# Kernel optimization log

Hardware: AMD Instinct MI355X
Metric: run time of the kernel (lower is better)

The kernel has to match this reference:

```python
import jax, jax.numpy as jnp
import numpy as np

B, LQ, LK = 4, 2048, 2048
DQ, DC = 1024, 1024
H, DH = 16, 64
INNER = H * DH
LN_EPS = 1e-5
TAU_INIT = DH ** -0.5


def layernorm(x, w, b):
    mu = jnp.mean(x, axis=-1, keepdims=True)
    var = jnp.var(x, axis=-1, keepdims=True)
    return (x - mu) * jax.lax.rsqrt(var + LN_EPS) * w + b


def l2norm(x, eps=1e-12):
    # matches F.normalize(dim=-1): x / max(||x||, eps)
    n = jnp.sqrt(jnp.sum(x * x, axis=-1, keepdims=True))
    return x / jnp.maximum(n, eps)


def setup_inputs() -> dict:
    key = jax.random.key(0)
    ks = jax.random.split(key, 8)
    s = lambda d: (1.0 / np.sqrt(d)).astype(np.float32) if isinstance(d, np.ndarray) else np.float32(1.0 / np.sqrt(d))
    return {
        "x": jax.random.normal(ks[0], (B, LQ, DQ), jnp.float32),
        "context": jax.random.normal(ks[1], (B, LK, DC), jnp.float32),
        "key_padding_mask": jax.random.bernoulli(ks[2], 0.1, (B, LK)),
        "ln_q_w": jnp.ones((DQ,), jnp.float32),
        "ln_q_b": jnp.zeros((DQ,), jnp.float32),
        "ln_ctx_w": jnp.ones((DC,), jnp.float32),
        "ln_ctx_b": jnp.zeros((DC,), jnp.float32),
        "Wq": jax.random.normal(ks[3], (DQ, INNER), jnp.float32) * s(DQ),
        "Wk": jax.random.normal(ks[4], (DC, INNER), jnp.float32) * s(DC),
        "Wv": jax.random.normal(ks[5], (DC, INNER), jnp.float32) * s(DC),
        "Wo": jax.random.normal(ks[6], (INNER, DQ), jnp.float32) * s(INNER),
        "tau": jnp.float32(TAU_INIT),
    }


def reference(x, context, key_padding_mask, ln_q_w, ln_q_b, ln_ctx_w, ln_ctx_b, Wq, Wk, Wv, Wo, tau):
    q_in = layernorm(x, ln_q_w, ln_q_b)
    kv_in = layernorm(context, ln_ctx_w, ln_ctx_b)
    q = (q_in @ Wq).reshape(B, LQ, H, DH)   # [B,Lq,H,Dh]
    k = (kv_in @ Wk).reshape(B, LK, H, DH)
    v = (kv_in @ Wv).reshape(B, LK, H, DH)
    q = l2norm(q)
    k = l2norm(k)
    scores = jnp.einsum('bqhd,bkhd->bhqk', q, k) / (tau + 1e-6)
    scores = jnp.where(key_padding_mask[:, None, None, :], -jnp.inf, scores)
    attn = jax.nn.softmax(scores, axis=-1)
    out = jnp.einsum('bhqk,bkhd->bqhd', attn, v).reshape(B, LQ, INNER)
    return out @ Wo
```

## Files before the change

### kernel.cpp

```cpp
#include <hip/hip_runtime.h>

typedef unsigned short u16;
typedef __bf16 bf16x8 __attribute__((ext_vector_type(8)));
typedef short s16x4 __attribute__((ext_vector_type(4)));
typedef float f32x4 __attribute__((ext_vector_type(4)));

__device__ __forceinline__ u16 f2bf(float f) {
  unsigned u = __float_as_uint(f);
  unsigned r = u + 0x7fffu + ((u >> 16) & 1u);
  return (u16)(r >> 16);
}

__device__ __forceinline__ unsigned cvt_pk(float a, float b) {
  unsigned r;
  asm("v_cvt_pk_bf16_f32 %0, %1, %2" : "=v"(r) : "v"(a), "v"(b));
  return r;
}

__device__ __forceinline__ void async_cp16(const void* g, void* l) {
  __builtin_amdgcn_global_load_lds((__attribute__((address_space(1))) void*)g,
                                   (__attribute__((address_space(3))) void*)l,
                                   16, 0, 0);
}

#define MFMA32(a, b, c) __builtin_amdgcn_mfma_f32_16x16x32_bf16(a, b, c, 0, 0, 0)

#if __has_builtin(__builtin_amdgcn_mfma_f32_16x16x16bf16_1k)
#define MFMA16(a, b, c) __builtin_amdgcn_mfma_f32_16x16x16bf16_1k(a, b, c, 0, 0, 0)
#else
__device__ __forceinline__ f32x4 mfma16_fb(s16x4 a, s16x4 b, f32x4 c) {
  asm("v_mfma_f32_16x16x16_bf16 %0, %1, %2, %0" : "+v"(c) : "v"(a), "v"(b));
  return c;
}
#define MFMA16(a, b, c) mfma16_fb(a, b, c)
#endif

__global__ __launch_bounds__(256)
void ln_cast(const float* __restrict__ X, const float* __restrict__ W,
             const float* __restrict__ Bv, u16* __restrict__ Y) {
  __shared__ float red[8];
  const int row = blockIdx.x, t = threadIdx.x;
  const int wave = t >> 6, lane = t & 63;
  const float4 v = ((const float4*)(X + (size_t)row * 1024))[t];
  float s  = v.x + v.y + v.z + v.w;
  float ss = v.x*v.x + v.y*v.y + v.z*v.z + v.w*v.w;
#pragma unroll
  for (int m = 32; m; m >>= 1) { s += __shfl_xor(s, m, 64); ss += __shfl_xor(ss, m, 64); }
  if (lane == 0) { red[wave] = s; red[4 + wave] = ss; }
  __syncthreads();
  float S  = red[0] + red[1] + red[2] + red[3];
  float SS = red[4] + red[5] + red[6] + red[7];
  float mu  = S * (1.0f / 1024.0f);
  float var = SS * (1.0f / 1024.0f) - mu * mu;
  float rstd = rsqrtf(var + 1e-5f);
  const float4 wv = ((const float4*)W)[t];
  const float4 bv = ((const float4*)Bv)[t];
  ushort4 o;
  o.x = f2bf((v.x - mu) * rstd * wv.x + bv.x);
  o.y = f2bf((v.y - mu) * rstd * wv.y + bv.y);
  o.z = f2bf((v.z - mu) * rstd * wv.z + bv.z);
  o.w = f2bf((v.w - mu) * rstd * wv.w + bv.w);
  ((ushort4*)(Y + (size_t)row * 1024))[t] = o;
}

__global__ __launch_bounds__(256)
void wtrans(const float* __restrict__ W, u16* __restrict__ WT) {
  __shared__ float t[64][65];
  const int k0 = blockIdx.y * 64, n0 = blockIdx.x * 64;
  const int lr = threadIdx.x >> 4, lc = threadIdx.x & 15;
#pragma unroll
  for (int r = 0; r < 4; ++r) {
    int row = r * 16 + lr;
    float4 v = *(const float4*)(W + (size_t)(k0 + row) * 1024 + n0 + lc * 4);
    t[row][lc*4+0] = v.x; t[row][lc*4+1] = v.y; t[row][lc*4+2] = v.z; t[row][lc*4+3] = v.w;
  }
  __syncthreads();
#pragma unroll
  for (int r = 0; r < 4; ++r) {
    int n = r * 16 + lr;
    ushort4 o;
    o.x = f2bf(t[lc*4+0][n]); o.y = f2bf(t[lc*4+1][n]);
    o.z = f2bf(t[lc*4+2][n]); o.w = f2bf(t[lc*4+3][n]);
    *(ushort4*)(WT + (size_t)(n0 + n) * 1024 + k0 + lc * 4) = o;
  }
}

__global__ __launch_bounds__(256)
void vtrans(const float* __restrict__ V, u16* __restrict__ VT) {
  __shared__ float t[64][65];
  const int b = blockIdx.z, h = blockIdx.y, kk0 = blockIdx.x * 64;
  const int lr = threadIdx.x >> 4, lc = threadIdx.x & 15;
#pragma unroll
  for (int r = 0; r < 4; ++r) {
    int row = r * 16 + lr;
    float4 v = *(const float4*)(V + (size_t)(b * 2048 + kk0 + row) * 1024 + h * 64 + lc * 4);
    t[row][lc*4+0] = v.x; t[row][lc*4+1] = v.y; t[row][lc*4+2] = v.z; t[row][lc*4+3] = v.w;
  }
  __syncthreads();
#pragma unroll
  for (int r = 0; r < 4; ++r) {
    int d = r * 16 + lr;
    ushort4 o;
    o.x = f2bf(t[lc*4+0][d]); o.y = f2bf(t[lc*4+1][d]);
    o.z = f2bf(t[lc*4+2][d]); o.w = f2bf(t[lc*4+3][d]);
    *(ushort4*)(VT + ((size_t)(b * 16 + h) * 64 + d) * 2048 + kk0 + lc * 4) = o;
  }
}

__global__ __launch_bounds__(256, 2)
void gemm_bt(const u16* __restrict__ A, const u16* __restrict__ Bt,
             float* __restrict__ C, int M, int N, int K) {
  __shared__ __align__(16) u16 As[128 * 64];
  __shared__ __align__(16) u16 Bs[128 * 64];
  const int tid = threadIdx.x;
  const int wave = tid >> 6, lane = tid & 63;
  const int quad = lane >> 4, l15 = lane & 15;
  const int m0 = blockIdx.y * 128, n0 = blockIdx.x * 128;
  const int wm = (wave >> 1) * 64, wn = (wave & 1) * 64;
  const int srow = lane >> 3, scol = (lane & 7) * 8;

  const f32x4 fz = {0.f, 0.f, 0.f, 0.f};
  f32x4 acc[4][4];
#pragma unroll
  for (int i = 0; i < 4; ++i)
#pragma unroll
    for (int j = 0; j < 4; ++j) acc[i][j] = fz;

  for (int kt = 0; kt < K; kt += 64) {
    __syncthreads();
#pragma unroll
    for (int r = 0; r < 4; ++r) {
      const int c = r * 4 + wave;
      const int row = c * 8 + srow;
      async_cp16(A  + (size_t)(m0 + row) * K + kt + scol, (char*)As + c * 1024);
      async_cp16(Bt + (size_t)(n0 + row) * K + kt + scol, (char*)Bs + c * 1024);
    }
    __syncthreads();
#pragma unroll
    for (int ks = 0; ks < 2; ++ks) {
      bf16x8 af[4], bfr[4];
#pragma unroll
      for (int i = 0; i < 4; ++i)
        af[i] = *(const bf16x8*)(const void*)(As + (wm + i * 16 + l15) * 64 + ks * 32 + quad * 8);
#pragma unroll
      for (int j = 0; j < 4; ++j)
        bfr[j] = *(const bf16x8*)(const void*)(Bs + (wn + j * 16 + l15) * 64 + ks * 32 + quad * 8);
#pragma unroll
      for (int i = 0; i < 4; ++i)
#pragma unroll
        for (int j = 0; j < 4; ++j)
          acc[i][j] = MFMA32(af[i], bfr[j], acc[i][j]);
    }
  }
#pragma unroll
  for (int i = 0; i < 4; ++i)
#pragma unroll
    for (int j = 0; j < 4; ++j)
#pragma unroll
      for (int e = 0; e < 4; ++e) {
        int row = m0 + wm + i * 16 + quad * 4 + e;
        int col = n0 + wn + j * 16 + l15;
        C[(size_t)row * N + col] = acc[i][j][e];
      }
}

__global__ __launch_bounds__(256, 2)
void gemm_l2n(const u16* __restrict__ A, const u16* __restrict__ Bt,
              u16* __restrict__ Y, const float* __restrict__ taup, int scaled) {
  __shared__ __align__(16) u16 As[128 * 64];
  __shared__ __align__(16) u16 Bs[128 * 64];
  const int tid = threadIdx.x;
  const int wave = tid >> 6, lane = tid & 63;
  const int quad = lane >> 4, l15 = lane & 15;
  const int m0 = blockIdx.y * 128, n0 = blockIdx.x * 128;
  const int wm = (wave >> 1) * 64, wn = (wave & 1) * 64;
  const int srow = lane >> 3, scol = (lane & 7) * 8;
  const int K = 1024, N = 1024;

  const f32x4 fz = {0.f, 0.f, 0.f, 0.f};
  f32x4 acc[4][4];
#pragma unroll
  for (int i = 0; i < 4; ++i)
#pragma unroll
    for (int j = 0; j < 4; ++j) acc[i][j] = fz;

  for (int kt = 0; kt < K; kt += 64) {
    __syncthreads();
#pragma unroll
    for (int r = 0; r < 4; ++r) {
      const int c = r * 4 + wave;
      const int row = c * 8 + srow;
      async_cp16(A  + (size_t)(m0 + row) * K + kt + scol, (char*)As + c * 1024);
      async_cp16(Bt + (size_t)(n0 + row) * K + kt + scol, (char*)Bs + c * 1024);
    }
    __syncthreads();
#pragma unroll
    for (int ks = 0; ks < 2; ++ks) {
      bf16x8 af[4], bfr[4];
#pragma unroll
      for (int i = 0; i < 4; ++i)
        af[i] = *(const bf16x8*)(const void*)(As + (wm + i * 16 + l15) * 64 + ks * 32 + quad * 8);
#pragma unroll
      for (int j = 0; j < 4; ++j)
        bfr[j] = *(const bf16x8*)(const void*)(Bs + (wn + j * 16 + l15) * 64 + ks * 32 + quad * 8);
#pragma unroll
      for (int i = 0; i < 4; ++i)
#pragma unroll
        for (int j = 0; j < 4; ++j)
          acc[i][j] = MFMA32(af[i], bfr[j], acc[i][j]);
    }
  }
  const float tsc = scaled ? 1.44269504f / (taup[0] + 1e-6f) : 1.0f;
#pragma unroll
  for (int i = 0; i < 4; ++i)
#pragma unroll
    for (int e = 0; e < 4; ++e) {
      float ss = 0.f;
#pragma unroll
      for (int j = 0; j < 4; ++j) ss = fmaf(acc[i][j][e], acc[i][j][e], ss);
      ss += __shfl_xor(ss, 1, 64); ss += __shfl_xor(ss, 2, 64);
      ss += __shfl_xor(ss, 4, 64); ss += __shfl_xor(ss, 8, 64);
      float sc = tsc / fmaxf(sqrtf(ss), 1e-12f);
      int row = m0 + wm + i * 16 + quad * 4 + e;
#pragma unroll
      for (int j = 0; j < 4; ++j)
        Y[(size_t)row * N + n0 + wn + j * 16 + l15] = f2bf(acc[i][j][e] * sc);
    }
}

__global__ __launch_bounds__(256, 2)
void flash_attn6(const u16* __restrict__ Qb, const u16* __restrict__ Kb,
                 const u16* __restrict__ Vt, const int* __restrict__ mask,
                 u16* __restrict__ Ob) {
  __shared__ __align__(16) u16 QPs[256 * 64];
  __shared__ __align__(16) u16 Ks[64 * 64];
  __shared__ __align__(16) u16 Vs[64 * 64];
  __shared__ __align__(16) u16 Msb[2048];
  const int tid = threadIdx.x, w = tid >> 6, lane = tid & 63;
  const int quad = lane >> 4, l15 = lane & 15;
  const int b = blockIdx.z, h = blockIdx.y, q0 = blockIdx.x * 256;
  const int srow = lane >> 3;
  const int scolX = ((lane & 7) ^ srow) * 8;
  const int fsw = ((l15 & 7) << 4);

#pragma unroll
  for (int r = 0; r < 8; ++r) {
    int c = w * 8 + r;
    async_cp16(Qb + (size_t)(b * 2048 + q0 + c * 8 + srow) * 1024 + h * 64 + scolX,
               (char*)QPs + c * 1024);
  }
  {
    const int* mp = mask + b * 2048 + tid * 8;
    int4 ma = *(const int4*)mp;
    int4 mb = *(const int4*)(mp + 4);
    ushort4 o0, o1;
    o0.x = ma.x ? 0xFF7Fu : 0u; o0.y = ma.y ? 0xFF7Fu : 0u;
    o0.z = ma.z ? 0xFF7Fu : 0u; o0.w = ma.w ? 0xFF7Fu : 0u;
    o1.x = mb.x ? 0xFF7Fu : 0u; o1.y = mb.y ? 0xFF7Fu : 0u;
    o1.z = mb.z ? 0xFF7Fu : 0u; o1.w = mb.w ? 0xFF7Fu : 0u;
    *(ushort4*)(Msb + tid * 8)     = o0;
    *(ushort4*)(Msb + tid * 8 + 4) = o1;
  }
  __syncthreads();

  bf16x8 aq[4][2];
#pragma unroll
  for (int i = 0; i < 4; ++i)
#pragma unroll
    for (int ks = 0; ks < 2; ++ks)
      aq[i][ks] = *(const bf16x8*)(const void*)(
          (const char*)QPs + (w * 64 + i * 16 + l15) * 128 + (((ks * 4 + quad) << 4) ^ fsw));

  const f32x4 fz = {0.f, 0.f, 0.f, 0.f};
  f32x4 o[4][4];
  float rs[4] = {0.f, 0.f, 0.f, 0.f};
#pragma unroll
  for (int dt = 0; dt < 4; ++dt)
#pragma unroll
    for (int i = 0; i < 4; ++i) o[dt][i] = fz;

  for (int kt = 0; kt < 2048; kt += 64) {
    __syncthreads();
#pragma unroll
    for (int r = 0; r < 2; ++r) {
      int c = w * 2 + r;
      async_cp16(Kb + (size_t)(b * 2048 + kt + c * 8 + srow) * 1024 + h * 64 + scolX,
                 (char*)Ks + c * 1024);
      async_cp16(Vt + ((size_t)(b * 16 + h) * 64 + c * 8 + srow) * 2048 + kt + scolX,
                 (char*)Vs + c * 1024);
    }
    __syncthreads();

    bf16x8 kb[4][2];
#pragma unroll
    for (int kkt = 0; kkt < 4; ++kkt)
#pragma unroll
      for (int ks = 0; ks < 2; ++ks)
        kb[kkt][ks] = *(const bf16x8*)(const void*)(
            (const char*)Ks + (kkt * 16 + l15) * 128 + (((ks * 4 + quad) << 4) ^ fsw));

#pragma unroll
    for (int kkt = 0; kkt < 4; ++kkt) {
      s16x4 mbv = *(const s16x4*)(Msb + kt + kkt * 16 + quad * 4);
      f32x4 bias;
#pragma unroll
      for (int e = 0; e < 4; ++e)
        bias[e] = __uint_as_float(((unsigned)(u16)mbv[e]) << 16);

      s16x4 pf[4];
#pragma unroll
      for (int i = 0; i < 4; ++i) {
        f32x4 st = MFMA32(kb[kkt][0], aq[i][0], bias);
        st = MFMA32(kb[kkt][1], aq[i][1], st);
        float p0 = exp2f(st[0]), p1 = exp2f(st[1]);
        float p2 = exp2f(st[2]), p3 = exp2f(st[3]);
        rs[i] += (p0 + p1) + (p2 + p3);
        union { unsigned u[2]; s16x4 s; } pk;
        pk.u[0] = cvt_pk(p0, p1);
        pk.u[1] = cvt_pk(p2, p3);
        pf[i] = pk.s;
      }
      __builtin_amdgcn_s_setprio(1);
#pragma unroll
      for (int dt = 0; dt < 4; ++dt) {
        s16x4 va = *(const s16x4*)(const void*)(
            (const char*)Vs + (dt * 16 + l15) * 128 + ((kkt * 32 + quad * 8) ^ fsw));
#pragma unroll
        for (int i = 0; i < 4; ++i)
          o[dt][i] = MFMA16(va, pf[i], o[dt][i]);
      }
      __builtin_amdgcn_s_setprio(0);
    }
  }

  float inv[4];
#pragma unroll
  for (int i = 0; i < 4; ++i) {
    float v = rs[i];
    v += __shfl_xor(v, 16, 64);
    v += __shfl_xor(v, 32, 64);
    inv[i] = 1.0f / v;
  }

  u16* strip = QPs + w * 64 * 64;
#pragma unroll
  for (int dt = 0; dt < 4; ++dt)
#pragma unroll
    for (int i = 0; i < 4; ++i) {
      union { unsigned u[2]; s16x4 s; } pk;
      pk.u[0] = cvt_pk(o[dt][i][0] * inv[i], o[dt][i][1] * inv[i]);
      pk.u[1] = cvt_pk(o[dt][i][2] * inv[i], o[dt][i][3] * inv[i]);
      *(s16x4*)(void*)((char*)strip + (i * 16 + l15) * 128 + ((dt * 32 + quad * 8) ^ fsw)) = pk.s;
    }
#pragma unroll
  for (int pass = 0; pass < 8; ++pass) {
    int row = pass * 8 + (lane >> 3), oct = lane & 7;
    int4 v = *(const int4*)(const void*)((const char*)strip + row * 128 + ((oct ^ (row & 7)) << 4));
    *(int4*)(Ob + (size_t)(b * 2048 + q0 + w * 64 + row) * 1024 + h * 64 + oct * 8) = v;
  }
}

extern "C" void kernel_launch(void* const* d_in, const int* in_sizes, int n_in,
                              void* d_out, int out_size, void* d_ws, size_t ws_size,
                              hipStream_t stream) {
  const float* x    = (const float*)d_in[0];
  const float* ctx  = (const float*)d_in[1];
  const int*   mask = (const int*)d_in[2];
  const float* lnqw = (const float*)d_in[3];
  const float* lnqb = (const float*)d_in[4];
  const float* lncw = (const float*)d_in[5];
  const float* lncb = (const float*)d_in[6];
  const float* Wq   = (const float*)d_in[7];
  const float* Wk   = (const float*)d_in[8];
  const float* Wv   = (const float*)d_in[9];
  const float* Wo   = (const float*)d_in[10];
  const float* tau  = (const float*)d_in[11];
  float* out = (float*)d_out;
  char* ws = (char*)d_ws;
  const size_t MB = 1024 * 1024;

  u16* qin  = (u16*)(ws + 0 * MB);
  u16* kvin = (u16*)(ws + 16 * MB);
  u16* WqT  = (u16*)(ws + 32 * MB);
  u16* WkT  = (u16*)(ws + 34 * MB);
  u16* WvT  = (u16*)(ws + 36 * MB);
  u16* WoT  = (u16*)(ws + 38 * MB);
  u16* qbf  = (u16*)(ws + 40 * MB);
  u16* kbf  = (u16*)(ws + 56 * MB);
  u16* vT   = (u16*)(ws + 72 * MB);
  float* scr = out;
  u16* attn = qin;

  ln_cast<<<8192, 256, 0, stream>>>(x,   lnqw, lnqb, qin);
  ln_cast<<<8192, 256, 0, stream>>>(ctx, lncw, lncb, kvin);
  wtrans<<<dim3(16, 16), 256, 0, stream>>>(Wq, WqT);
  wtrans<<<dim3(16, 16), 256, 0, stream>>>(Wk, WkT);
  wtrans<<<dim3(16, 16), 256, 0, stream>>>(Wv, WvT);
  wtrans<<<dim3(16, 16), 256, 0, stream>>>(Wo, WoT);

  gemm_l2n<<<dim3(8, 64), 256, 0, stream>>>(qin,  WqT, qbf, tau, 1);
  gemm_l2n<<<dim3(8, 64), 256, 0, stream>>>(kvin, WkT, kbf, tau, 0);

  gemm_bt<<<dim3(8, 64), 256, 0, stream>>>(kvin, WvT, scr, 8192, 1024, 1024);
  vtrans<<<dim3(32, 16, 4), 256, 0, stream>>>(scr, vT);

  flash_attn6<<<dim3(8, 16, 4), 256, 0, stream>>>(qbf, kbf, vT, mask, attn);

  gemm_bt<<<dim3(8, 64), 256, 0, stream>>>(attn, WoT, out, 8192, 1024, 1024);
}
```

Measured before the change: 394.5 us.

## Double-buffer LDS tiles in GEMM and flash-attention kernels to overlap loads

The projection GEMMs and the attention kernel now keep two LDS buffers per operand. Each loop iteration issues the async global-to-LDS copy for the next tile before computing on the current one. This leaves a single barrier per iteration instead of two, so global load latency can hide behind MFMA work. In exchange, LDS use per block doubles for the operand tiles, which could limit occupancy. Correctness also depends on the barrier waiting for the async LDS copies to complete.

After: 404.2 us. +2.5%, slower.

```diff
diff --git a/kernel.cpp b/kernel.cpp
--- a/kernel.cpp
+++ b/kernel.cpp
@@ -110,8 +110,8 @@
 __global__ __launch_bounds__(256, 2)
 void gemm_bt(const u16* __restrict__ A, const u16* __restrict__ Bt,
              float* __restrict__ C, int M, int N, int K) {
-  __shared__ __align__(16) u16 As[128 * 64];
-  __shared__ __align__(16) u16 Bs[128 * 64];
+  __shared__ __align__(16) u16 As[2][128 * 64];
+  __shared__ __align__(16) u16 Bs[2][128 * 64];
   const int tid = threadIdx.x;
   const int wave = tid >> 6, lane = tid & 63;
   const int quad = lane >> 4, l15 = lane & 15;
@@ -126,31 +126,43 @@
 #pragma unroll
     for (int j = 0; j < 4; ++j) acc[i][j] = fz;
 
+#pragma unroll
+  for (int r = 0; r < 4; ++r) {
+    const int c = r * 4 + wave;
+    const int row = c * 8 + srow;
+    async_cp16(A  + (size_t)(m0 + row) * K + scol, (char*)As[0] + c * 1024);
+    async_cp16(Bt + (size_t)(n0 + row) * K + scol, (char*)Bs[0] + c * 1024);
+  }
+  __syncthreads();
+
+  int cur = 0;
   for (int kt = 0; kt < K; kt += 64) {
-    __syncthreads();
-#pragma unroll
-    for (int r = 0; r < 4; ++r) {
-      const int c = r * 4 + wave;
-      const int row = c * 8 + srow;
-      async_cp16(A  + (size_t)(m0 + row) * K + kt + scol, (char*)As + c * 1024);
-      async_cp16(Bt + (size_t)(n0 + row) * K + kt + scol, (char*)Bs + c * 1024);
-    }
-    __syncthreads();
+    if (kt + 64 < K) {
+#pragma unroll
+      for (int r = 0; r < 4; ++r) {
+        const int c = r * 4 + wave;
+        const int row = c * 8 + srow;
+        async_cp16(A  + (size_t)(m0 + row) * K + kt + 64 + scol, (char*)As[cur ^ 1] + c * 1024);
+        async_cp16(Bt + (size_t)(n0 + row) * K + kt + 64 + scol, (char*)Bs[cur ^ 1] + c * 1024);
+      }
+    }
 #pragma unroll
     for (int ks = 0; ks < 2; ++ks) {
       bf16x8 af[4], bfr[4];
 #pragma unroll
       for (int i = 0; i < 4; ++i)
-        af[i] = *(const bf16x8*)(const void*)(As + (wm + i * 16 + l15) * 64 + ks * 32 + quad * 8);
+        af[i] = *(const bf16x8*)(const void*)(As[cur] + (wm + i * 16 + l15) * 64 + ks * 32 + quad * 8);
 #pragma unroll
       for (int j = 0; j < 4; ++j)
-        bfr[j] = *(const bf16x8*)(const void*)(Bs + (wn + j * 16 + l15) * 64 + ks * 32 + quad * 8);
+        bfr[j] = *(const bf16x8*)(const void*)(Bs[cur] + (wn + j * 16 + l15) * 64 + ks * 32 + quad * 8);
 #pragma unroll
       for (int i = 0; i < 4; ++i)
 #pragma unroll
         for (int j = 0; j < 4; ++j)
           acc[i][j] = MFMA32(af[i], bfr[j], acc[i][j]);
     }
+    __syncthreads();
+    cur ^= 1;
   }
 #pragma unroll
   for (int i = 0; i < 4; ++i)
@@ -167,8 +179,8 @@
 __global__ __launch_bounds__(256, 2)
 void gemm_l2n(const u16* __restrict__ A, const u16* __restrict__ Bt,
               u16* __restrict__ Y, const float* __restrict__ taup, int scaled) {
-  __shared__ __align__(16) u16 As[128 * 64];
-  __shared__ __align__(16) u16 Bs[128 * 64];
+  __shared__ __align__(16) u16 As[2][128 * 64];
+  __shared__ __align__(16) u16 Bs[2][128 * 64];
   const int tid = threadIdx.x;
   const int wave = tid >> 6, lane = tid & 63;
   const int quad = lane >> 4, l15 = lane & 15;
@@ -184,31 +196,43 @@
 #pragma unroll
     for (int j = 0; j < 4; ++j) acc[i][j] = fz;
 
+#pragma unroll
+  for (int r = 0; r < 4; ++r) {
+    const int c = r * 4 + wave;
+    const int row = c * 8 + srow;
+    async_cp16(A  + (size_t)(m0 + row) * K + scol, (char*)As[0] + c * 1024);
+    async_cp16(Bt + (size_t)(n0 + row) * K + scol, (char*)Bs[0] + c * 1024);
+  }
+  __syncthreads();
+
+  int cur = 0;
   for (int kt = 0; kt < K; kt += 64) {
-    __syncthreads();
-#pragma unroll
-    for (int r = 0; r < 4; ++r) {
-      const int c = r * 4 + wave;
-      const int row = c * 8 + srow;
-      async_cp16(A  + (size_t)(m0 + row) * K + kt + scol, (char*)As + c * 1024);
-      async_cp16(Bt + (size_t)(n0 + row) * K + kt + scol, (char*)Bs + c * 1024);
-    }
-    __syncthreads();
+    if (kt + 64 < K) {
+#pragma unroll
+      for (int r = 0; r < 4; ++r) {
+        const int c = r * 4 + wave;
+        const int row = c * 8 + srow;
+        async_cp16(A  + (size_t)(m0 + row) * K + kt + 64 + scol, (char*)As[cur ^ 1] + c * 1024);
+        async_cp16(Bt + (size_t)(n0 + row) * K + kt + 64 + scol, (char*)Bs[cur ^ 1] + c * 1024);
+      }
+    }
 #pragma unroll
     for (int ks = 0; ks < 2; ++ks) {
       bf16x8 af[4], bfr[4];
 #pragma unroll
       for (int i = 0; i < 4; ++i)
-        af[i] = *(const bf16x8*)(const void*)(As + (wm + i * 16 + l15) * 64 + ks * 32 + quad * 8);
+        af[i] = *(const bf16x8*)(const void*)(As[cur] + (wm + i * 16 + l15) * 64 + ks * 32 + quad * 8);
 #pragma unroll
       for (int j = 0; j < 4; ++j)
-        bfr[j] = *(const bf16x8*)(const void*)(Bs + (wn + j * 16 + l15) * 64 + ks * 32 + quad * 8);
+        bfr[j] = *(const bf16x8*)(const void*)(Bs[cur] + (wn + j * 16 + l15) * 64 + ks * 32 + quad * 8);
 #pragma unroll
       for (int i = 0; i < 4; ++i)
 #pragma unroll
         for (int j = 0; j < 4; ++j)
           acc[i][j] = MFMA32(af[i], bfr[j], acc[i][j]);
     }
+    __syncthreads();
+    cur ^= 1;
   }
   const float tsc = scaled ? 1.44269504f / (taup[0] + 1e-6f) : 1.0f;
 #pragma unroll
@@ -229,12 +253,12 @@
 }
 
 __global__ __launch_bounds__(256, 2)
-void flash_attn6(const u16* __restrict__ Qb, const u16* __restrict__ Kb,
+void flash_attn7(const u16* __restrict__ Qb, const u16* __restrict__ Kb,
                  const u16* __restrict__ Vt, const int* __restrict__ mask,
                  u16* __restrict__ Ob) {
   __shared__ __align__(16) u16 QPs[256 * 64];
-  __shared__ __align__(16) u16 Ks[64 * 64];
-  __shared__ __align__(16) u16 Vs[64 * 64];
+  __shared__ __align__(16) u16 Ks[2][64 * 64];
+  __shared__ __align__(16) u16 Vs[2][64 * 64];
   __shared__ __align__(16) u16 Msb[2048];
   const int tid = threadIdx.x, w = tid >> 6, lane = tid & 63;
   const int quad = lane >> 4, l15 = lane & 15;
@@ -248,6 +272,14 @@
     int c = w * 8 + r;
     async_cp16(Qb + (size_t)(b * 2048 + q0 + c * 8 + srow) * 1024 + h * 64 + scolX,
                (char*)QPs + c * 1024);
+  }
+#pragma unroll
+  for (int r = 0; r < 2; ++r) {
+    int c = w * 2 + r;
+    async_cp16(Kb + (size_t)(b * 2048 + c * 8 + srow) * 1024 + h * 64 + scolX,
+               (char*)Ks[0] + c * 1024);
+    async_cp16(Vt + ((size_t)(b * 16 + h) * 64 + c * 8 + srow) * 2048 + scolX,
+               (char*)Vs[0] + c * 1024);
   }
   {
     const int* mp = mask + b * 2048 + tid * 8;
@@ -279,17 +311,18 @@
 #pragma unroll
     for (int i = 0; i < 4; ++i) o[dt][i] = fz;
 
+  int cur = 0;
   for (int kt = 0; kt < 2048; kt += 64) {
-    __syncthreads();
-#pragma unroll
-    for (int r = 0; r < 2; ++r) {
-      int c = w * 2 + r;
-      async_cp16(Kb + (size_t)(b * 2048 + kt + c * 8 + srow) * 1024 + h * 64 + scolX,
-                 (char*)Ks + c * 1024);
-      async_cp16(Vt + ((size_t)(b * 16 + h) * 64 + c * 8 + srow) * 2048 + kt + scolX,
-                 (char*)Vs + c * 1024);
-    }
-    __syncthreads();
+    if (kt + 64 < 2048) {
+#pragma unroll
+      for (int r = 0; r < 2; ++r) {
+        int c = w * 2 + r;
+        async_cp16(Kb + (size_t)(b * 2048 + kt + 64 + c * 8 + srow) * 1024 + h * 64 + scolX,
+                   (char*)Ks[cur ^ 1] + c * 1024);
+        async_cp16(Vt + ((size_t)(b * 16 + h) * 64 + c * 8 + srow) * 2048 + kt + 64 + scolX,
+                   (char*)Vs[cur ^ 1] + c * 1024);
+      }
+    }
 
     bf16x8 kb[4][2];
 #pragma unroll
@@ -297,7 +330,7 @@
 #pragma unroll
       for (int ks = 0; ks < 2; ++ks)
         kb[kkt][ks] = *(const bf16x8*)(const void*)(
-            (const char*)Ks + (kkt * 16 + l15) * 128 + (((ks * 4 + quad) << 4) ^ fsw));
+            (const char*)Ks[cur] + (kkt * 16 + l15) * 128 + (((ks * 4 + quad) << 4) ^ fsw));
 
 #pragma unroll
     for (int kkt = 0; kkt < 4; ++kkt) {
@@ -324,13 +357,15 @@
 #pragma unroll
       for (int dt = 0; dt < 4; ++dt) {
         s16x4 va = *(const s16x4*)(const void*)(
-            (const char*)Vs + (dt * 16 + l15) * 128 + ((kkt * 32 + quad * 8) ^ fsw));
+            (const char*)Vs[cur] + (dt * 16 + l15) * 128 + ((kkt * 32 + quad * 8) ^ fsw));
 #pragma unroll
         for (int i = 0; i < 4; ++i)
           o[dt][i] = MFMA16(va, pf[i], o[dt][i]);
       }
       __builtin_amdgcn_s_setprio(0);
     }
+    __syncthreads();
+    cur ^= 1;
   }
 
   float inv[4];
@@ -404,7 +439,7 @@
   gemm_bt<<<dim3(8, 64), 256, 0, stream>>>(kvin, WvT, scr, 8192, 1024, 1024);
   vtrans<<<dim3(32, 16, 4), 256, 0, stream>>>(scr, vT);
 
-  flash_attn6<<<dim3(8, 16, 4), 256, 0, stream>>>(qbf, kbf, vT, mask, attn);
+  flash_attn7<<<dim3(8, 16, 4), 256, 0, stream>>>(qbf, kbf, vT, mask, attn);
 
   gemm_bt<<<dim3(8, 64), 256, 0, stream>>>(attn, WoT, out, 8192, 1024, 1024);
 }
```

## Double-buffer K/V tiles in attention, use fp32 mask bias and fast exp2

Applied to the files above, without the earlier changes.

The attention kernel now prefetches the next K/V tile into a second LDS buffer while the current tile is being computed, replacing the two barriers per iteration with one. The mask bias is stored as fp32 in LDS, so it is read directly and no longer unpacked from bf16. exp2f is swapped for the hardware exp2 builtin. The added LDS for the double buffers and the mask may reduce occupancy, and there is a possible race because there is no wait on the async loads before the tile is read.

Measured after the change: 366.6 us. -7.1%, faster.

```diff
diff --git a/kernel.cpp b/kernel.cpp
--- a/kernel.cpp
+++ b/kernel.cpp
@@ -16,6 +16,12 @@
   asm("v_cvt_pk_bf16_f32 %0, %1, %2" : "=v"(r) : "v"(a), "v"(b));
   return r;
 }
+
+#if __has_builtin(__builtin_amdgcn_exp2f)
+#define EXP2(x) __builtin_amdgcn_exp2f(x)
+#else
+#define EXP2(x) exp2f(x)
+#endif
 
 __device__ __forceinline__ void async_cp16(const void* g, void* l) {
   __builtin_amdgcn_global_load_lds((__attribute__((address_space(1))) void*)g,
@@ -229,13 +235,13 @@
 }
 
 __global__ __launch_bounds__(256, 2)
-void flash_attn6(const u16* __restrict__ Qb, const u16* __restrict__ Kb,
+void flash_attn9(const u16* __restrict__ Qb, const u16* __restrict__ Kb,
                  const u16* __restrict__ Vt, const int* __restrict__ mask,
                  u16* __restrict__ Ob) {
   __shared__ __align__(16) u16 QPs[256 * 64];
-  __shared__ __align__(16) u16 Ks[64 * 64];
-  __shared__ __align__(16) u16 Vs[64 * 64];
-  __shared__ __align__(16) u16 Msb[2048];
+  __shared__ __align__(16) u16 Ks[2][64 * 64];
+  __shared__ __align__(16) u16 Vs[2][64 * 64];
+  __shared__ __align__(16) float Msf[2048];
   const int tid = threadIdx.x, w = tid >> 6, lane = tid & 63;
   const int quad = lane >> 4, l15 = lane & 15;
   const int b = blockIdx.z, h = blockIdx.y, q0 = blockIdx.x * 256;
@@ -249,17 +255,25 @@
     async_cp16(Qb + (size_t)(b * 2048 + q0 + c * 8 + srow) * 1024 + h * 64 + scolX,
                (char*)QPs + c * 1024);
   }
+#pragma unroll
+  for (int r = 0; r < 2; ++r) {
+    int c = w * 2 + r;
+    async_cp16(Kb + (size_t)(b * 2048 + c * 8 + srow) * 1024 + h * 64 + scolX,
+               (char*)Ks[0] + c * 1024);
+    async_cp16(Vt + ((size_t)(b * 16 + h) * 64 + c * 8 + srow) * 2048 + scolX,
+               (char*)Vs[0] + c * 1024);
+  }
   {
     const int* mp = mask + b * 2048 + tid * 8;
     int4 ma = *(const int4*)mp;
     int4 mb = *(const int4*)(mp + 4);
-    ushort4 o0, o1;
-    o0.x = ma.x ? 0xFF7Fu : 0u; o0.y = ma.y ? 0xFF7Fu : 0u;
-    o0.z = ma.z ? 0xFF7Fu : 0u; o0.w = ma.w ? 0xFF7Fu : 0u;
-    o1.x = mb.x ? 0xFF7Fu : 0u; o1.y = mb.y ? 0xFF7Fu : 0u;
-    o1.z = mb.z ? 0xFF7Fu : 0u; o1.w = mb.w ? 0xFF7Fu : 0u;
-    *(ushort4*)(Msb + tid * 8)     = o0;
-    *(ushort4*)(Msb + tid * 8 + 4) = o1;
+    float4 o0, o1;
+    o0.x = ma.x ? -3.0e38f : 0.f; o0.y = ma.y ? -3.0e38f : 0.f;
+    o0.z = ma.z ? -3.0e38f : 0.f; o0.w = ma.w ? -3.0e38f : 0.f;
+    o1.x = mb.x ? -3.0e38f : 0.f; o1.y = mb.y ? -3.0e38f : 0.f;
+    o1.z = mb.z ? -3.0e38f : 0.f; o1.w = mb.w ? -3.0e38f : 0.f;
+    *(float4*)(Msf + tid * 8)     = o0;
+    *(float4*)(Msf + tid * 8 + 4) = o1;
   }
   __syncthreads();
 
@@ -279,17 +293,18 @@
 #pragma unroll
     for (int i = 0; i < 4; ++i) o[dt][i] = fz;
 
+  int cur = 0;
   for (int kt = 0; kt < 2048; kt += 64) {
-    __syncthreads();
-#pragma unroll
-    for (int r = 0; r < 2; ++r) {
-      int c = w * 2 + r;
-      async_cp16(Kb + (size_t)(b * 2048 + kt + c * 8 + srow) * 1024 + h * 64 + scolX,
-                 (char*)Ks + c * 1024);
-      async_cp16(Vt + ((size_t)(b * 16 + h) * 64 + c * 8 + srow) * 2048 + kt + scolX,
-                 (char*)Vs + c * 1024);
-    }
-    __syncthreads();
+    if (kt + 64 < 2048) {
+#pragma unroll
+      for (int r = 0; r < 2; ++r) {
+        int c = w * 2 + r;
+        async_cp16(Kb + (size_t)(b * 2048 + kt + 64 + c * 8 + srow) * 1024 + h * 64 + scolX,
+                   (char*)Ks[cur ^ 1] + c * 1024);
+        async_cp16(Vt + ((size_t)(b * 16 + h) * 64 + c * 8 + srow) * 2048 + kt + 64 + scolX,
+                   (char*)Vs[cur ^ 1] + c * 1024);
+      }
+    }
 
     bf16x8 kb[4][2];
 #pragma unroll
@@ -297,23 +312,19 @@
 #pragma unroll
       for (int ks = 0; ks < 2; ++ks)
         kb[kkt][ks] = *(const bf16x8*)(const void*)(
-            (const char*)Ks + (kkt * 16 + l15) * 128 + (((ks * 4 + quad) << 4) ^ fsw));
+            (const char*)Ks[cur] + (kkt * 16 + l15) * 128 + (((ks * 4 + quad) << 4) ^ fsw));
 
 #pragma unroll
     for (int kkt = 0; kkt < 4; ++kkt) {
-      s16x4 mbv = *(const s16x4*)(Msb + kt + kkt * 16 + quad * 4);
-      f32x4 bias;
-#pragma unroll
-      for (int e = 0; e < 4; ++e)
-        bias[e] = __uint_as_float(((unsigned)(u16)mbv[e]) << 16);
+      f32x4 bias = *(const f32x4*)(Msf + kt + kkt * 16 + quad * 4);
 
       s16x4 pf[4];
 #pragma unroll
       for (int i = 0; i < 4; ++i) {
         f32x4 st = MFMA32(kb[kkt][0], aq[i][0], bias);
         st = MFMA32(kb[kkt][1], aq[i][1], st);
-        float p0 = exp2f(st[0]), p1 = exp2f(st[1]);
-        float p2 = exp2f(st[2]), p3 = exp2f(st[3]);
+        float p0 = EXP2(st[0]), p1 = EXP2(st[1]);
+        float p2 = EXP2(st[2]), p3 = EXP2(st[3]);
         rs[i] += (p0 + p1) + (p2 + p3);
         union { unsigned u[2]; s16x4 s; } pk;
         pk.u[0] = cvt_pk(p0, p1);
@@ -324,13 +335,15 @@
 #pragma unroll
       for (int dt = 0; dt < 4; ++dt) {
         s16x4 va = *(const s16x4*)(const void*)(
-            (const char*)Vs + (dt * 16 + l15) * 128 + ((kkt * 32 + quad * 8) ^ fsw));
+            (const char*)Vs[cur] + (dt * 16 + l15) * 128 + ((kkt * 32 + quad * 8) ^ fsw));
 #pragma unroll
         for (int i = 0; i < 4; ++i)
           o[dt][i] = MFMA16(va, pf[i], o[dt][i]);
       }
       __builtin_amdgcn_s_setprio(0);
     }
+    __syncthreads();
+    cur ^= 1;
   }
 
   float inv[4];
@@ -404,7 +417,7 @@
   gemm_bt<<<dim3(8, 64), 256, 0, stream>>>(kvin, WvT, scr, 8192, 1024, 1024);
   vtrans<<<dim3(32, 16, 4), 256, 0, stream>>>(scr, vT);
 
-  flash_attn6<<<dim3(8, 16, 4), 256, 0, stream>>>(qbf, kbf, vT, mask, attn);
+  flash_attn9<<<dim3(8, 16, 4), 256, 0, stream>>>(qbf, kbf, vT, mask, attn);
 
   gemm_bt<<<dim3(8, 64), 256, 0, stream>>>(attn, WoT, out, 8192, 1024, 1024);
 }
```
